# Performance work log

Hardware: AMD Instinct MI355X
Metric: run time of the kernel (lower is better)

The kernel has to match this reference:

```python
import jax, jax.numpy as jnp
import numpy as np
import math

NEG = -10000.0  # module uses -10000, not -inf


def setup_inputs() -> dict:
    key = jax.random.key(0)
    k1, k2, k3 = jax.random.split(key, 3)
    B, Sq, Sk, H, Hkv, D = 2, 2048, 2048, 16, 4, 64
    q = jax.random.normal(k1, (B, Sq, H, D), dtype=jnp.float32)
    kv = jax.random.normal(k2, (B, Sk, 2, Hkv, D), dtype=jnp.float32)
    key_padding_mask = jax.random.randint(k3, (B, Sk), 0, 2) > 0  # True = valid key
    return {"q": q, "kv": kv, "key_padding_mask": key_padding_mask}


def reference(q, kv, key_padding_mask):
    B, Sq, H, D = q.shape
    Sk, Hkv = kv.shape[1], kv.shape[3]
    if Hkv != H:
        # einops repeat '... hkv d -> ... (hkv g) d': each kv head repeated g times contiguously
        kv = jnp.repeat(kv, H // Hkv, axis=3)
    k, v = kv[:, :, 0], kv[:, :, 1]  # [B, Sk, H, D] each
    scale = 1.0 / math.sqrt(D)
    scores = jnp.einsum('bthd,bshd->bhts', q, k * scale)  # [B, H, Sq, Sk]
    # key padding: additive 0 where valid, -10000 where padded
    pad = jnp.where(key_padding_mask, 0.0, NEG).astype(scores.dtype)
    scores = scores + pad[:, None, None, :]
    # causal mask: cols > rows + Sk - Sq gets replaced (not added) with -10000
    rows = jnp.arange(Sq)[:, None]
    cols = jnp.arange(Sk)[None, :]
    causal_mask = cols > rows + (Sk - Sq)
    scores = jnp.where(causal_mask, NEG, scores)
    attention = jax.nn.softmax(scores, axis=-1).astype(v.dtype)
    # dropout p=0.0 -> identity
    output = jnp.einsum('bhts,bshd->bthd', attention, v)  # [B, Sq, H, D]
    return output
```

## Files before the change

### kernel.cpp

```cpp
#include <hip/hip_runtime.h>
#include <math.h>


typedef __bf16 bf16x4 __attribute__((ext_vector_type(4)));
typedef __bf16 bf16x8 __attribute__((ext_vector_type(8)));
typedef float floatx4 __attribute__((ext_vector_type(4)));
typedef short shortx4 __attribute__((ext_vector_type(4)));

#define SQ 2048
#define SK 2048
#define H_ 16
#define HKV 4
#define D_ 64
#define QT 64
#define KT 64
#define KVROW 512
#define NEGV (-10000.0f)
#define QSCL 0.18033688f
#define EBIAS 17.3123405f
#define IMG_BYTES (256 * 16384)

static __device__ __forceinline__ floatx4 mfma16(bf16x4 a, bf16x4 b, floatx4 c) {
#if __has_builtin(__builtin_amdgcn_mfma_f32_16x16x16bf16_1k)
    return __builtin_amdgcn_mfma_f32_16x16x16bf16_1k(
        __builtin_bit_cast(shortx4, a), __builtin_bit_cast(shortx4, b), c, 0, 0, 0);
#else
    floatx4 d;
    asm("v_mfma_f32_16x16x16_bf16 %0, %1, %2, %3"
        : "=v"(d) : "v"(a), "v"(b), "v"(c));
    return d;
#endif
}

static __device__ __forceinline__ void gload16(const void* g, void* l) {
    __builtin_amdgcn_global_load_lds(
        (const __attribute__((address_space(1))) unsigned int*)g,
        (__attribute__((address_space(3))) unsigned int*)l, 16, 0, 0);
}

__global__ __launch_bounds__(256)
void prep_kernel(const float* __restrict__ kv, const int* __restrict__ mask,
                 char* __restrict__ imgs, unsigned long long* __restrict__ kept)
{
    __shared__ alignas(16) __bf16 Vl[64][64];
    const int tid = threadIdx.x;
    const int bid = (int)blockIdx.x;
    const int kt = bid & 31, hkv = (bid >> 5) & 3, b = bid >> 7;
    const float* kvb = kv + ((size_t)b * SK + kt * KT) * KVROW + hkv * D_;
    const float* vvb = kvb + HKV * D_;
    char* img = imgs + ((size_t)bid << 14);

    const int r  = tid >> 2;
    const int gg = tid & 3;

    {
        const float* p = kvb + (size_t)r * KVROW + gg * 16;
        float4 f0 = *(const float4*)(p + 0), f1 = *(const float4*)(p + 4);
        float4 f2 = *(const float4*)(p + 8), f3 = *(const float4*)(p + 12);
        bf16x8 c0 = { (__bf16)f0.x, (__bf16)f0.y, (__bf16)f0.z, (__bf16)f0.w,
                      (__bf16)f1.x, (__bf16)f1.y, (__bf16)f1.z, (__bf16)f1.w };
        bf16x8 c1 = { (__bf16)f2.x, (__bf16)f2.y, (__bf16)f2.z, (__bf16)f2.w,
                      (__bf16)f3.x, (__bf16)f3.y, (__bf16)f3.z, (__bf16)f3.w };
        const int xo = (r & 7) << 4;
        *(bf16x8*)(img + r * 128 + (((gg * 2 + 0) * 16) ^ xo)) = c0;
        *(bf16x8*)(img + r * 128 + (((gg * 2 + 1) * 16) ^ xo)) = c1;
    }
    {
        const float* p = vvb + (size_t)r * KVROW + gg * 16;
        float4 f0 = *(const float4*)(p + 0), f1 = *(const float4*)(p + 4);
        float4 f2 = *(const float4*)(p + 8), f3 = *(const float4*)(p + 12);
        float t[16] = { f0.x, f0.y, f0.z, f0.w, f1.x, f1.y, f1.z, f1.w,
                        f2.x, f2.y, f2.z, f2.w, f3.x, f3.y, f3.z, f3.w };
#pragma unroll
        for (int j = 0; j < 16; ++j)
            Vl[gg * 16 + j][r] = (__bf16)t[j];
    }
    __syncthreads();
#pragma unroll
    for (int i = 0; i < 2; ++i) {
        const int c = tid * 2 + i, rr = c >> 3, g = c & 7;
        bf16x8 v = *(const bf16x8*)&Vl[rr][g * 8];
        *(bf16x8*)(img + 8192 + rr * 128 + ((g * 16) ^ ((rr & 7) << 4))) = v;
    }
    if (tid < 64) {
        int m = mask[b * SK + kt * KT + tid];
        unsigned long long kk = __ballot(m != 0);
        if (tid == 0 && hkv == 0) kept[b * 32 + kt] = kk;
    }
}

__global__ __launch_bounds__(256, 5)
void attn_kernel(const float* __restrict__ q,
                 const float* __restrict__ kv,
                 const int* __restrict__ mask,
                 float* __restrict__ out,
                 float* __restrict__ ws)
{
    __shared__ alignas(16) union {
        struct {
            __bf16 K[2][KT * D_];
            __bf16 V[2][D_ * KT];
        } m;
        struct {
            float fpart[4][64];
            float fw[4][64];
            int   s_first;
        } f;
    } sh;

    const int tid  = threadIdx.x;
    const int wave = tid >> 6;
    const int lane = tid & 63;
    const int col  = lane & 15;
    const int quad = lane >> 4;

    if (blockIdx.x < 32) {
        const int bh = (int)blockIdx.x;
        const int b = bh >> 4, h = bh & 15, hkv = h >> 2;
        if (tid == 0) sh.f.s_first = SK;
        __syncthreads();
        int local = SK;
        for (int s = tid; s < SK; s += 256)
            if (mask[b * SK + s]) local = min(local, s);
        atomicMin(&sh.f.s_first, local);
        __syncthreads();
        const int nfirst = sh.f.s_first;
        if (nfirst == 0) return;

        const float* kvb = kv + (size_t)b * SK * KVROW + hkv * D_;
        const float* vvb = kvb + HKV * D_;
        {
            float a0=0,a1=0,a2=0,a3=0,a4=0,a5=0,a6=0,a7=0;
            const int s0 = wave * 512;
            for (int s = s0; s < s0 + 512; s += 8) {
                a0 += vvb[(size_t)(s+0)*KVROW + lane];
                a1 += vvb[(size_t)(s+1)*KVROW + lane];
                a2 += vvb[(size_t)(s+2)*KVROW + lane];
                a3 += vvb[(size_t)(s+3)*KVROW + lane];
                a4 += vvb[(size_t)(s+4)*KVROW + lane];
                a5 += vvb[(size_t)(s+5)*KVROW + lane];
                a6 += vvb[(size_t)(s+6)*KVROW + lane];
                a7 += vvb[(size_t)(s+7)*KVROW + lane];
            }
            sh.f.fpart[wave][lane] = ((a0+a1)+(a2+a3)) + ((a4+a5)+(a6+a7));
        }
        __syncthreads();
        const float vtotal = sh.f.fpart[0][lane] + sh.f.fpart[1][lane]
                           + sh.f.fpart[2][lane] + sh.f.fpart[3][lane];

        for (int R = wave; R < nfirst; R += 4) {
            const float* qrow = q + (((size_t)b * SQ + R) * H_ + h) * D_;
            float mymax = -3.4e38f;
            for (int s = lane; s <= R; s += 64) {
                const float* kp = kvb + (size_t)s * KVROW;
                float dt = 0.f;
                for (int d = 0; d < D_; ++d) dt += qrow[d] * kp[d];
                mymax = fmaxf(mymax, dt * 0.125f + NEGV);
            }
#pragma unroll
            for (int off = 32; off >= 1; off >>= 1)
                mymax = fmaxf(mymax, __shfl_xor(mymax, off, 64));
            const float M = (R < SK - 1) ? fmaxf(mymax, NEGV) : mymax;
            float lsum = 0.f, oacc = 0.f, pref = 0.f;
            for (int s0 = 0; s0 <= R; s0 += 64) {
                int s = s0 + lane;
                float w = 0.f;
                if (s <= R) {
                    const float* kp = kvb + (size_t)s * KVROW;
                    float dt = 0.f;
                    for (int d = 0; d < D_; ++d) dt += qrow[d] * kp[d];
                    w = __expf(dt * 0.125f + NEGV - M);
                    lsum += w;
                }
                sh.f.fw[wave][lane] = w;
                const int nk = (R - s0 + 1 < 64) ? (R - s0 + 1) : 64;
                for (int j = 0; j < nk; ++j) {
                    const float vj = vvb[(size_t)(s0 + j) * KVROW + lane];
                    oacc += sh.f.fw[wave][j] * vj;
                    pref += vj;
                }
            }
#pragma unroll
            for (int off = 32; off >= 1; off >>= 1)
                lsum += __shfl_xor(lsum, off, 64);
            const float wn   = __expf(NEGV - M);
            const float ltot = lsum + wn * (float)(SK - 1 - R);
            out[(((size_t)b * SQ + R) * H_ + h) * D_ + lane] =
                (oacc + wn * (vtotal - pref)) / ltot;
        }
        return;
    }

    const int id = (int)blockIdx.x - 32;
    const int bh = id & 31;
    const int y  = id >> 5;
    const int kg = y >> 3, jj = y & 7;
    const int qt = (kg == 0) ? 31 - jj : (kg == 1) ? jj : (kg == 2) ? 23 - jj : 8 + jj;
    const int b = bh >> 4, h = bh & 15, hkv = h >> 2;
    const int qw = qt * QT + wave * 16;

    const char* imgb = (const char*)ws;
    const unsigned long long* keptarr =
        (const unsigned long long*)(imgb + IMG_BYTES);
    const char* timg0 = imgb + ((size_t)((b * 4 + hkv) * 32) << 14);

    bf16x8 aq[2];
    {
        const int row = qw + col;
        const float* qp = q + (((size_t)b * SQ + row) * H_ + h) * D_ + quad * 8;
#pragma unroll
        for (int kc = 0; kc < 2; ++kc) {
            const float* p = qp + kc * 32;
#pragma unroll
            for (int j = 0; j < 8; ++j) aq[kc][j] = (__bf16)(p[j] * QSCL);
        }
    }

    bf16x4 vone4;
#pragma unroll
    for (int j = 0; j < 4; ++j) vone4[j] = (__bf16)1.0f;

    floatx4 o[4];
    floatx4 l_acc = (floatx4){0.f, 0.f, 0.f, 0.f};
#pragma unroll
    for (int dj = 0; dj < 4; ++dj) o[dj] = (floatx4){0.f, 0.f, 0.f, 0.f};

    const int c7 = col & 7;
    const int xo = c7 << 4;

    auto gstage = [&](int kt, int bb) {
        const char* img = timg0 + ((size_t)kt << 14);
        const char* gsK = img + wave * 1024 + lane * 16;
        const char* gsV = img + 8192 + wave * 1024 + lane * 16;
        char* ldK = (char*)&sh.m.K[bb][0] + wave * 1024;
        char* ldV = (char*)&sh.m.V[bb][0] + wave * 1024;
        gload16(gsK,        ldK);
        gload16(gsK + 4096, ldK + 4096);
        gload16(gsV,        ldV);
        gload16(gsV + 4096, ldV + 4096);
    };

    const int k1 = qt + 1;
    gstage(0, 0);
    int cur = 0;
    for (int kt = 0; kt < k1; ++kt) {
        __syncthreads();
        if (kt + 1 < k1) gstage(kt + 1, cur ^ 1);
        const unsigned long long kept = keptarr[b * 32 + kt];

        const char* Kb = (const char*)&sh.m.K[cur][0];
        floatx4 c[4];
        __builtin_amdgcn_s_setprio(1);
#pragma unroll
        for (int kj = 0; kj < 4; ++kj) {
            c[kj] = (floatx4){0.f, 0.f, 0.f, 0.f};
#pragma unroll
            for (int kc = 0; kc < 2; ++kc) {
                bf16x8 ak = *(const bf16x8*)(Kb + (kj * 16 + col) * 128
                                                + ((((kc * 4 + quad) ^ c7) << 4)));
                c[kj] = __builtin_amdgcn_mfma_f32_16x16x32_bf16(ak, aq[kc], c[kj], 0, 0, 0);
            }
        }
        __builtin_amdgcn_s_setprio(0);

        const unsigned long long kq = kept >> (quad * 4);
        bf16x4 pk[4];
        if (kt == qt) {
            const int tcl = wave * 16 + col - quad * 4;
#pragma unroll
            for (int kj = 0; kj < 4; ++kj) {
#pragma unroll
                for (int r = 0; r < 4; ++r) {
                    float p = __builtin_amdgcn_exp2f(c[kj][r] - EBIAS);
                    const bool keep = ((kq >> (kj * 16 + r)) & 1ull)
                                    && (kj * 16 + r <= tcl);
                    pk[kj][r] = (__bf16)(keep ? p : 0.f);
                }
            }
        } else {
#pragma unroll
            for (int kj = 0; kj < 4; ++kj) {
#pragma unroll
                for (int r = 0; r < 4; ++r) {
                    float p = __builtin_amdgcn_exp2f(c[kj][r] - EBIAS);
                    const bool keep = (kq >> (kj * 16 + r)) & 1ull;
                    pk[kj][r] = (__bf16)(keep ? p : 0.f);
                }
            }
        }

        const char* Vb = (const char*)&sh.m.V[cur][0];
        __builtin_amdgcn_s_setprio(1);
#pragma unroll
        for (int kj = 0; kj < 4; ++kj)
            l_acc = mfma16(pk[kj], vone4, l_acc);
#pragma unroll
        for (int dj = 0; dj < 4; ++dj)
#pragma unroll
            for (int kj = 0; kj < 4; ++kj) {
                bf16x4 bv = *(const bf16x4*)(Vb + (dj * 16 + col) * 128
                                                + ((kj * 32 + quad * 8) ^ xo));
                o[dj] = mfma16(pk[kj], bv, o[dj]);
            }
        __builtin_amdgcn_s_setprio(0);
        cur ^= 1;
    }

#pragma unroll
    for (int r = 0; r < 4; ++r) {
        const float l = l_acc[r];
        if (l > 0.f) {
            const float inv = 1.0f / l;
            const int row = qw + quad * 4 + r;
            float* op = out + (((size_t)b * SQ + row) * H_ + h) * D_ + col;
#pragma unroll
            for (int dj = 0; dj < 4; ++dj)
                op[dj * 16] = o[dj][r] * inv;
        }
    }
}

extern "C" void kernel_launch(void* const* d_in, const int* in_sizes, int n_in,
                              void* d_out, int out_size, void* d_ws, size_t ws_size,
                              hipStream_t stream) {
    const float* q   = (const float*)d_in[0];
    const float* kv  = (const float*)d_in[1];
    const int* mask  = (const int*)d_in[2];
    float* out       = (float*)d_out;
    char* imgs = (char*)d_ws;
    unsigned long long* kept = (unsigned long long*)(imgs + IMG_BYTES);
    prep_kernel<<<dim3(256), 256, 0, stream>>>(kv, mask, imgs, kept);
    attn_kernel<<<dim3(32 + 1024), 256, 0, stream>>>(q, kv, mask, out, (float*)d_ws);
}
```

Measured before the change: 111.2 us.

## Process two query heads sharing a KV head per block to reuse K/V tiles

Each attention block now handles two query heads that share the same GQA KV head. Every K/V tile staged into shared memory is reused for both heads, which halves the grid and the global-to-LDS traffic per head. In exchange each thread holds twice the accumulators and Q fragments, so launch bounds drop from 5 to 4 blocks per CU. With half as many blocks, load balance across CUs for the causal workload also becomes coarser.

```diff
diff --git a/kernel.cpp b/kernel.cpp
--- a/kernel.cpp
+++ b/kernel.cpp
@@ -89,7 +89,7 @@
     }
 }
 
-__global__ __launch_bounds__(256, 5)
+__global__ __launch_bounds__(256, 4)
 void attn_kernel(const float* __restrict__ q,
                  const float* __restrict__ kv,
                  const int* __restrict__ mask,
@@ -192,11 +192,12 @@
     }
 
     const int id = (int)blockIdx.x - 32;
-    const int bh = id & 31;
-    const int y  = id >> 5;
+    const int combo = id & 15;
+    const int y  = id >> 4;
     const int kg = y >> 3, jj = y & 7;
     const int qt = (kg == 0) ? 31 - jj : (kg == 1) ? jj : (kg == 2) ? 23 - jj : 8 + jj;
-    const int b = bh >> 4, h = bh & 15, hkv = h >> 2;
+    const int b = combo >> 3, hkv = (combo >> 1) & 3, hp = combo & 1;
+    const int h0 = hkv * 4 + hp * 2;
     const int qw = qt * QT + wave * 16;
 
     const char* imgb = (const char*)ws;
@@ -204,15 +205,16 @@
         (const unsigned long long*)(imgb + IMG_BYTES);
     const char* timg0 = imgb + ((size_t)((b * 4 + hkv) * 32) << 14);
 
-    bf16x8 aq[2];
-    {
+    bf16x8 aq[2][2];
+#pragma unroll
+    for (int g = 0; g < 2; ++g) {
         const int row = qw + col;
-        const float* qp = q + (((size_t)b * SQ + row) * H_ + h) * D_ + quad * 8;
+        const float* qp = q + (((size_t)b * SQ + row) * H_ + (h0 + g)) * D_ + quad * 8;
 #pragma unroll
         for (int kc = 0; kc < 2; ++kc) {
             const float* p = qp + kc * 32;
 #pragma unroll
-            for (int j = 0; j < 8; ++j) aq[kc][j] = (__bf16)(p[j] * QSCL);
+            for (int j = 0; j < 8; ++j) aq[g][kc][j] = (__bf16)(p[j] * QSCL);
         }
     }
 
@@ -220,10 +222,14 @@
 #pragma unroll
     for (int j = 0; j < 4; ++j) vone4[j] = (__bf16)1.0f;
 
-    floatx4 o[4];
-    floatx4 l_acc = (floatx4){0.f, 0.f, 0.f, 0.f};
-#pragma unroll
-    for (int dj = 0; dj < 4; ++dj) o[dj] = (floatx4){0.f, 0.f, 0.f, 0.f};
+    floatx4 o[2][4];
+    floatx4 l_acc[2];
+#pragma unroll
+    for (int g = 0; g < 2; ++g) {
+        l_acc[g] = (floatx4){0.f, 0.f, 0.f, 0.f};
+#pragma unroll
+        for (int dj = 0; dj < 4; ++dj) o[g][dj] = (floatx4){0.f, 0.f, 0.f, 0.f};
+    }
 
     const int c7 = col & 7;
     const int xo = c7 << 4;
@@ -249,32 +255,36 @@
         const unsigned long long kept = keptarr[b * 32 + kt];
 
         const char* Kb = (const char*)&sh.m.K[cur][0];
-        floatx4 c[4];
+        floatx4 c0[4], c1[4];
         __builtin_amdgcn_s_setprio(1);
 #pragma unroll
         for (int kj = 0; kj < 4; ++kj) {
-            c[kj] = (floatx4){0.f, 0.f, 0.f, 0.f};
+            c0[kj] = (floatx4){0.f, 0.f, 0.f, 0.f};
+            c1[kj] = (floatx4){0.f, 0.f, 0.f, 0.f};
 #pragma unroll
             for (int kc = 0; kc < 2; ++kc) {
                 bf16x8 ak = *(const bf16x8*)(Kb + (kj * 16 + col) * 128
                                                 + ((((kc * 4 + quad) ^ c7) << 4)));
-                c[kj] = __builtin_amdgcn_mfma_f32_16x16x32_bf16(ak, aq[kc], c[kj], 0, 0, 0);
+                c0[kj] = __builtin_amdgcn_mfma_f32_16x16x32_bf16(ak, aq[0][kc], c0[kj], 0, 0, 0);
+                c1[kj] = __builtin_amdgcn_mfma_f32_16x16x32_bf16(ak, aq[1][kc], c1[kj], 0, 0, 0);
             }
         }
         __builtin_amdgcn_s_setprio(0);
 
         const unsigned long long kq = kept >> (quad * 4);
-        bf16x4 pk[4];
+        bf16x4 pk0[4], pk1[4];
         if (kt == qt) {
             const int tcl = wave * 16 + col - quad * 4;
 #pragma unroll
             for (int kj = 0; kj < 4; ++kj) {
 #pragma unroll
                 for (int r = 0; r < 4; ++r) {
-                    float p = __builtin_amdgcn_exp2f(c[kj][r] - EBIAS);
                     const bool keep = ((kq >> (kj * 16 + r)) & 1ull)
                                     && (kj * 16 + r <= tcl);
-                    pk[kj][r] = (__bf16)(keep ? p : 0.f);
+                    float p0 = __builtin_amdgcn_exp2f(c0[kj][r] - EBIAS);
+                    float p1 = __builtin_amdgcn_exp2f(c1[kj][r] - EBIAS);
+                    pk0[kj][r] = (__bf16)(keep ? p0 : 0.f);
+                    pk1[kj][r] = (__bf16)(keep ? p1 : 0.f);
                 }
             }
         } else {
@@ -282,9 +292,11 @@
             for (int kj = 0; kj < 4; ++kj) {
 #pragma unroll
                 for (int r = 0; r < 4; ++r) {
-                    float p = __builtin_amdgcn_exp2f(c[kj][r] - EBIAS);
                     const bool keep = (kq >> (kj * 16 + r)) & 1ull;
-                    pk[kj][r] = (__bf16)(keep ? p : 0.f);
+                    float p0 = __builtin_amdgcn_exp2f(c0[kj][r] - EBIAS);
+                    float p1 = __builtin_amdgcn_exp2f(c1[kj][r] - EBIAS);
+                    pk0[kj][r] = (__bf16)(keep ? p0 : 0.f);
+                    pk1[kj][r] = (__bf16)(keep ? p1 : 0.f);
                 }
             }
         }
@@ -292,32 +304,37 @@
         const char* Vb = (const char*)&sh.m.V[cur][0];
         __builtin_amdgcn_s_setprio(1);
 #pragma unroll
-        for (int kj = 0; kj < 4; ++kj)
-            l_acc = mfma16(pk[kj], vone4, l_acc);
+        for (int kj = 0; kj < 4; ++kj) {
+            l_acc[0] = mfma16(pk0[kj], vone4, l_acc[0]);
+            l_acc[1] = mfma16(pk1[kj], vone4, l_acc[1]);
+        }
 #pragma unroll
         for (int dj = 0; dj < 4; ++dj)
 #pragma unroll
             for (int kj = 0; kj < 4; ++kj) {
                 bf16x4 bv = *(const bf16x4*)(Vb + (dj * 16 + col) * 128
                                                 + ((kj * 32 + quad * 8) ^ xo));
-                o[dj] = mfma16(pk[kj], bv, o[dj]);
+                o[0][dj] = mfma16(pk0[kj], bv, o[0][dj]);
+                o[1][dj] = mfma16(pk1[kj], bv, o[1][dj]);
             }
         __builtin_amdgcn_s_setprio(0);
         cur ^= 1;
     }
 
 #pragma unroll
-    for (int r = 0; r < 4; ++r) {
-        const float l = l_acc[r];
-        if (l > 0.f) {
-            const float inv = 1.0f / l;
-            const int row = qw + quad * 4 + r;
-            float* op = out + (((size_t)b * SQ + row) * H_ + h) * D_ + col;
-#pragma unroll
-            for (int dj = 0; dj < 4; ++dj)
-                op[dj * 16] = o[dj][r] * inv;
-        }
-    }
+    for (int g = 0; g < 2; ++g)
+#pragma unroll
+        for (int r = 0; r < 4; ++r) {
+            const float l = l_acc[g][r];
+            if (l > 0.f) {
+                const float inv = 1.0f / l;
+                const int row = qw + quad * 4 + r;
+                float* op = out + (((size_t)b * SQ + row) * H_ + (h0 + g)) * D_ + col;
+#pragma unroll
+                for (int dj = 0; dj < 4; ++dj)
+                    op[dj * 16] = o[g][dj][r] * inv;
+            }
+        }
 }
 
 extern "C" void kernel_launch(void* const* d_in, const int* in_sizes, int n_in,
@@ -330,5 +347,5 @@
     char* imgs = (char*)d_ws;
     unsigned long long* kept = (unsigned long long*)(imgs + IMG_BYTES);
     prep_kernel<<<dim3(256), 256, 0, stream>>>(kv, mask, imgs, kept);
-    attn_kernel<<<dim3(32 + 1024), 256, 0, stream>>>(q, kv, mask, out, (float*)d_ws);
-}
+    attn_kernel<<<dim3(32 + 512), 256, 0, stream>>>(q, kv, mask, out, (float*)d_ws);
+}
```

Measured after the change: 121.8 us. 1.1x slower.
